# Performance work log

Measured on AMD Instinct MI355X. Metric: run time of the kernel, lower is better.

## Reference

```python
import jax, jax.numpy as jnp
import numpy as np

FEAT_STRIDE = 32  # 520 // 16
POOL = 7          # adaptive_avg_pool2d target (7,7)
C = 8             # channels consumed as (2 classes x 4 coords)


def setup_inputs() -> dict:
    key = jax.random.key(0)
    k1, k2, k3 = jax.random.split(key, 3)
    H = W = 1024
    conv_out = jax.random.normal(k1, (1, C, H, W), dtype=jnp.float32)
    n = 8192
    # sample pixel-space coords in [0, H*FEAT_STRIDE) and sort so min<=max per axis
    ys = jnp.sort(jax.random.randint(k2, (n, 2), 0, H * FEAT_STRIDE), axis=1)
    xs = jnp.sort(jax.random.randint(k3, (n, 2), 0, W * FEAT_STRIDE), axis=1)
    rois = jnp.stack([ys[:, 0], xs[:, 0], ys[:, 1], xs[:, 1]], axis=1).astype(jnp.int64)
    return {"conv_out": conv_out, "rois": rois}


def _adaptive_bounds(start, length):
    # PyTorch adaptive_avg_pool2d bin edges over [start, start+length)
    j = jnp.arange(POOL)
    lo = start + (j * length) // POOL
    hi = start + ((j + 1) * length + POOL - 1) // POOL  # ceil div
    return lo, hi


def _forward(conv_out, rois):
    r = rois // FEAT_STRIDE
    x = conv_out[0]  # [C, H, W]
    # summed-area table, padded so sat[:, y, x] = sum over [0:y, 0:x)
    sat = jnp.pad(jnp.cumsum(jnp.cumsum(x, axis=1), axis=2),
                  ((0, 0), (1, 0), (1, 0)))  # [C, H+1, W+1]

    def pool_one(roi):
        ymin, xmin = roi[0], roi[1]
        ymax, xmax = roi[2] + 1, roi[3] + 1  # exclusive ends
        ylo, yhi = _adaptive_bounds(ymin, ymax - ymin)
        xlo, xhi = _adaptive_bounds(xmin, xmax - xmin)
        # 7x7 bin sums via inclusion-exclusion on SAT -> [C,7,7]
        s = (sat[:, yhi[:, None], xhi[None, :]]
             - sat[:, ylo[:, None], xhi[None, :]]
             - sat[:, yhi[:, None], xlo[None, :]]
             + sat[:, ylo[:, None], xlo[None, :]])
        area = ((yhi - ylo)[:, None] * (xhi - xlo)[None, :]).astype(s.dtype)
        block7 = s / area                       # adaptive_avg_pool2d -> (7,7)
        return block7.mean(axis=(1, 2))         # adaptive_avg_pool2d -> (1,1), [C]

    pooled = jax.vmap(pool_one)(r)              # [n, C]
    return pooled.reshape(-1, 2, 4)


def reference(conv_out, rois):
    return _forward(conv_out, rois)
```

## Files before the change

### kernel.cpp

```cpp
#include <hip/hip_runtime.h>
#include <cstddef>
#include <cstdint>

#define SATW_PAD 1026
#define W8   8200
#define W8P  8208
#define NCH  8
#define STRIP 16
#define NSTRIP (W8P / STRIP)

__global__ __launch_bounds__(256) void rowscan_kernel(const float* __restrict__ in,
                                                      float* __restrict__ sat) {
    const int y    = blockIdx.x;
    const int t    = threadIdx.x;
    const int lane = t & 63;
    const int wv   = t >> 6;

    __shared__ float lds[NCH][1024];

    for (int k = 0; k < 2; ++k) {
        const int c = wv * 2 + k;
        const float4* r4 = (const float4*)(in + ((size_t)c * 1024 + y) * 1024);
        double chunkbase = 0.0;
#pragma unroll
        for (int j = 0; j < 4; ++j) {
            float4 a = r4[lane + 64 * j];
            double v0 = a.x, v1 = a.y, v2 = a.z, v3 = a.w;
            double s = v0 + v1 + v2 + v3;
            double ps = s;
#pragma unroll
            for (int off = 1; off < 64; off <<= 1) {
                double n = __shfl_up(ps, off, 64);
                if (lane >= off) ps += n;
            }
            double base = chunkbase + ps - s;
            double p0 = base + v0, p1 = p0 + v1, p2 = p1 + v2, p3 = p2 + v3;
            ((float4*)lds[c])[lane + 64 * j] =
                make_float4((float)p0, (float)p1, (float)p2, (float)p3);
            chunkbase += __shfl(ps, 63, 64);
        }
    }
    __syncthreads();

    float* orow = sat + (size_t)(y + 1) * W8P;
    for (int f4 = t; f4 < W8P / 4; f4 += 256) {
        int f = f4 * 4;
        float4 o;
        float* po = (float*)&o;
#pragma unroll
        for (int j = 0; j < 4; ++j) {
            int ff = f + j;
            int x = ff >> 3, c = ff & 7;
            po[j] = (x >= 1 && x <= 1024) ? lds[c][x - 1] : 0.0f;
        }
        ((float4*)orow)[f4] = o;
    }
}

__global__ __launch_bounds__(1024, 8) void colscan_block(float* __restrict__ sat) {
    const int t    = threadIdx.x;
    const int lane = t & 63;
    const int w    = t >> 6;
    const int rg   = lane >> 2;
    const int q    = lane & 3;
    const int c0   = blockIdx.x * STRIP + q * 4;

    float* p0 = sat + (size_t)(1 + w * 64 + rg * 4) * W8P + c0;

    float4 v[4];
#pragma unroll
    for (int k = 0; k < 4; ++k)
        v[k] = *(const float4*)(p0 + (size_t)k * W8P);

    double T0 = 0, T1 = 0, T2 = 0, T3 = 0;
#pragma unroll
    for (int k = 0; k < 4; ++k) {
        T0 += v[k].x; T1 += v[k].y; T2 += v[k].z; T3 += v[k].w;
    }

    double i0 = T0, i1 = T1, i2 = T2, i3 = T3;
#pragma unroll
    for (int s = 4; s <= 32; s <<= 1) {
        double a0 = __shfl_up(i0, s, 64), a1 = __shfl_up(i1, s, 64);
        double a2 = __shfl_up(i2, s, 64), a3 = __shfl_up(i3, s, 64);
        if (lane >= s) { i0 += a0; i1 += a1; i2 += a2; i3 += a3; }
    }
    double b0 = i0 - T0, b1 = i1 - T1, b2 = i2 - T2, b3 = i3 - T3;

    __shared__ double wt[16][4][4];
    if (lane >= 60) {
        wt[w][q][0] = i0; wt[w][q][1] = i1; wt[w][q][2] = i2; wt[w][q][3] = i3;
    }
    __syncthreads();
    for (int w2 = 0; w2 < w; ++w2) {
        b0 += wt[w2][q][0]; b1 += wt[w2][q][1];
        b2 += wt[w2][q][2]; b3 += wt[w2][q][3];
    }

#pragma unroll
    for (int k = 0; k < 4; ++k) {
        b0 += v[k].x; b1 += v[k].y; b2 += v[k].z; b3 += v[k].w;
        *(float4*)(p0 + (size_t)k * W8P) =
            make_float4((float)b0, (float)b1, (float)b2, (float)b3);
    }

    if (t < 4) {
        int cz = blockIdx.x * STRIP + t * 4;
        *(float4*)(sat + cz) = make_float4(0.f, 0.f, 0.f, 0.f);
    }
}

__global__ __launch_bounds__(256) void pool_kernel(const float* __restrict__ sat,
                                                   const int* __restrict__ rois,
                                                   float* __restrict__ out,
                                                   int n_roi) {
    int lane = threadIdx.x & 63;
    int roi  = (blockIdx.x * blockDim.x + threadIdx.x) >> 6;
    if (roi >= n_roi) return;

    const int4 rv = ((const int4*)rois)[roi];
    int ymin = rv.x >> 5;
    int xmin = rv.y >> 5;
    int Ly   = (rv.z >> 5) + 1 - ymin;
    int Lx   = (rv.w >> 5) + 1 - xmin;

    float acc[NCH];
#pragma unroll
    for (int c = 0; c < NCH; ++c) acc[c] = 0.0f;

    if (lane < 49) {
        int by = lane / 7;
        int bx = lane - by * 7;
        int ylo = ymin + (by * Ly) / 7;
        int yhi = ymin + ((by + 1) * Ly + 6) / 7;
        int xlo = xmin + (bx * Lx) / 7;
        int xhi = xmin + ((bx + 1) * Lx + 6) / 7;
        float inv = 1.0f / (float)((yhi - ylo) * (xhi - xlo));

        float4 a[2], b[2], c4[2], d[2];
        const float4* hh = (const float4*)(sat + ((size_t)yhi * SATW_PAD + xhi) * NCH);
        const float4* lh = (const float4*)(sat + ((size_t)ylo * SATW_PAD + xhi) * NCH);
        const float4* hl = (const float4*)(sat + ((size_t)yhi * SATW_PAD + xlo) * NCH);
        const float4* ll = (const float4*)(sat + ((size_t)ylo * SATW_PAD + xlo) * NCH);
        a[0] = hh[0]; a[1] = hh[1];
        b[0] = lh[0]; b[1] = lh[1];
        c4[0] = hl[0]; c4[1] = hl[1];
        d[0] = ll[0]; d[1] = ll[1];
        const float* fa = (const float*)a;
        const float* fb = (const float*)b;
        const float* fc = (const float*)c4;
        const float* fd = (const float*)d;
#pragma unroll
        for (int c = 0; c < NCH; ++c)
            acc[c] = (fa[c] - fb[c] - fc[c] + fd[c]) * inv;
    }

#pragma unroll
    for (int off = 32; off; off >>= 1) {
#pragma unroll
        for (int c = 0; c < NCH; ++c) acc[c] += __shfl_down(acc[c], off, 64);
    }

    if (lane == 0) {
        const float k = 1.0f / 49.0f;
        float4* po = (float4*)(out + (size_t)roi * NCH);
        po[0] = make_float4(acc[0] * k, acc[1] * k, acc[2] * k, acc[3] * k);
        po[1] = make_float4(acc[4] * k, acc[5] * k, acc[6] * k, acc[7] * k);
    }
}

extern "C" void kernel_launch(void* const* d_in, const int* in_sizes, int n_in,
                              void* d_out, int out_size, void* d_ws, size_t ws_size,
                              hipStream_t stream) {
    const float* conv = (const float*)d_in[0];
    const int*   rois = (const int*)d_in[1];
    float*       out  = (float*)d_out;
    int n_roi = in_sizes[1] / 4;

    float* sat = (float*)d_ws;

    rowscan_kernel<<<1024, 256, 0, stream>>>(conv, sat);
    colscan_block<<<NSTRIP, 1024, 0, stream>>>(sat);
    pool_kernel<<<(n_roi + 3) / 4, 256, 0, stream>>>(sat, rois, out, n_roi);
}
```

Measured before the change: 123.0 us.

## Replace column-scan kernel with three-pass band reduce/prefix/apply scan

```diff
diff --git a/kernel.cpp b/kernel.cpp
--- a/kernel.cpp
+++ b/kernel.cpp
@@ -1,13 +1,17 @@
 #include <hip/hip_runtime.h>
 #include <cstddef>
 #include <cstdint>
+
 
 #define SATW_PAD 1026
 #define W8   8200
 #define W8P  8208
 #define NCH  8
-#define STRIP 16
-#define NSTRIP (W8P / STRIP)
+
+#define NBAND 64
+#define BROWS 16
+#define CHUNK_F32 1024
+#define NCHUNK 9
 
 __global__ __launch_bounds__(256) void rowscan_kernel(const float* __restrict__ in,
                                                       float* __restrict__ sat) {
@@ -57,57 +61,98 @@
     }
 }
 
-__global__ __launch_bounds__(1024, 8) void colscan_block(float* __restrict__ sat) {
-    const int t    = threadIdx.x;
-    const int lane = t & 63;
-    const int w    = t >> 6;
-    const int rg   = lane >> 2;
-    const int q    = lane & 3;
-    const int c0   = blockIdx.x * STRIP + q * 4;
-
-    float* p0 = sat + (size_t)(1 + w * 64 + rg * 4) * W8P + c0;
-
-    float4 v[4];
-#pragma unroll
-    for (int k = 0; k < 4; ++k)
-        v[k] = *(const float4*)(p0 + (size_t)k * W8P);
-
-    double T0 = 0, T1 = 0, T2 = 0, T3 = 0;
-#pragma unroll
-    for (int k = 0; k < 4; ++k) {
-        T0 += v[k].x; T1 += v[k].y; T2 += v[k].z; T3 += v[k].w;
-    }
-
-    double i0 = T0, i1 = T1, i2 = T2, i3 = T3;
-#pragma unroll
-    for (int s = 4; s <= 32; s <<= 1) {
-        double a0 = __shfl_up(i0, s, 64), a1 = __shfl_up(i1, s, 64);
-        double a2 = __shfl_up(i2, s, 64), a3 = __shfl_up(i3, s, 64);
-        if (lane >= s) { i0 += a0; i1 += a1; i2 += a2; i3 += a3; }
-    }
-    double b0 = i0 - T0, b1 = i1 - T1, b2 = i2 - T2, b3 = i3 - T3;
-
-    __shared__ double wt[16][4][4];
-    if (lane >= 60) {
-        wt[w][q][0] = i0; wt[w][q][1] = i1; wt[w][q][2] = i2; wt[w][q][3] = i3;
-    }
-    __syncthreads();
-    for (int w2 = 0; w2 < w; ++w2) {
-        b0 += wt[w2][q][0]; b1 += wt[w2][q][1];
-        b2 += wt[w2][q][2]; b3 += wt[w2][q][3];
-    }
-
-#pragma unroll
-    for (int k = 0; k < 4; ++k) {
-        b0 += v[k].x; b1 += v[k].y; b2 += v[k].z; b3 += v[k].w;
-        *(float4*)(p0 + (size_t)k * W8P) =
-            make_float4((float)b0, (float)b1, (float)b2, (float)b3);
-    }
-
-    if (t < 4) {
-        int cz = blockIdx.x * STRIP + t * 4;
-        *(float4*)(sat + cz) = make_float4(0.f, 0.f, 0.f, 0.f);
-    }
+__global__ __launch_bounds__(256) void band_sum(const float* __restrict__ sat,
+                                                double* __restrict__ bsum) {
+    const int c = blockIdx.x;
+    const int b = blockIdx.y;
+    const int t = threadIdx.x;
+    const int col0 = c * CHUNK_F32 + t * 4;
+    if (col0 >= W8) return;
+
+    const float* p = sat + (size_t)(1 + b * BROWS) * W8P + col0;
+    float4 v[BROWS];
+#pragma unroll
+    for (int k = 0; k < BROWS; ++k)
+        v[k] = *(const float4*)(p + (size_t)k * W8P);
+
+    double s0 = 0, s1 = 0, s2 = 0, s3 = 0;
+#pragma unroll
+    for (int k = 0; k < BROWS; ++k) {
+        s0 += v[k].x; s1 += v[k].y; s2 += v[k].z; s3 += v[k].w;
+    }
+
+    double* o = bsum + (size_t)b * W8P + col0;
+    double2 lo, hi;
+    lo.x = s0; lo.y = s1; hi.x = s2; hi.y = s3;
+    *(double2*)o       = lo;
+    *((double2*)o + 1) = hi;
+}
+
+__global__ __launch_bounds__(64) void band_prefix(double* __restrict__ bsum) {
+    const int lane = threadIdx.x;
+    const int rg   = lane >> 3;
+    const int s    = lane & 7;
+    const size_t base = (size_t)blockIdx.x * 16 + (size_t)s * 2;
+
+    double2 v[8];
+#pragma unroll
+    for (int k = 0; k < 8; ++k)
+        v[k] = *(const double2*)(bsum + (size_t)(rg * 8 + k) * W8P + base);
+
+    double i0 = 0, i1 = 0;
+    double incl0[8], incl1[8];
+#pragma unroll
+    for (int k = 0; k < 8; ++k) {
+        i0 += v[k].x; i1 += v[k].y;
+        incl0[k] = i0; incl1[k] = i1;
+    }
+
+    double a0 = i0, a1 = i1;
+#pragma unroll
+    for (int off = 8; off <= 32; off <<= 1) {
+        double u0 = __shfl_up(a0, off, 64);
+        double u1 = __shfl_up(a1, off, 64);
+        if (lane >= off) { a0 += u0; a1 += u1; }
+    }
+    const double base0 = a0 - i0, base1 = a1 - i1;
+
+#pragma unroll
+    for (int k = 0; k < 8; ++k) {
+        double2 e;
+        e.x = base0 + incl0[k] - v[k].x;
+        e.y = base1 + incl1[k] - v[k].y;
+        *(double2*)(bsum + (size_t)(rg * 8 + k) * W8P + base) = e;
+    }
+}
+
+__global__ __launch_bounds__(256) void band_apply(float* __restrict__ sat,
+                                                  const double* __restrict__ bpre) {
+    const int c = blockIdx.x;
+    const int b = blockIdx.y;
+    const int t = threadIdx.x;
+    const int col0 = c * CHUNK_F32 + t * 4;
+    if (col0 >= W8) return;
+
+    const double* q = bpre + (size_t)b * W8P + col0;
+    double2 qlo = *(const double2*)q;
+    double2 qhi = *((const double2*)q + 1);
+    double a0 = qlo.x, a1 = qlo.y, a2 = qhi.x, a3 = qhi.y;
+
+    float* p = sat + (size_t)(1 + b * BROWS) * W8P + col0;
+    float4 v[BROWS];
+#pragma unroll
+    for (int k = 0; k < BROWS; ++k)
+        v[k] = *(const float4*)(p + (size_t)k * W8P);
+
+#pragma unroll
+    for (int k = 0; k < BROWS; ++k) {
+        a0 += v[k].x; a1 += v[k].y; a2 += v[k].z; a3 += v[k].w;
+        *(float4*)(p + (size_t)k * W8P) =
+            make_float4((float)a0, (float)a1, (float)a2, (float)a3);
+    }
+
+    if (b == 0)
+        *(float4*)(sat + col0) = make_float4(0.f, 0.f, 0.f, 0.f);
 }
 
 __global__ __launch_bounds__(256) void pool_kernel(const float* __restrict__ sat,
@@ -177,9 +222,12 @@
     float*       out  = (float*)d_out;
     int n_roi = in_sizes[1] / 4;
 
-    float* sat = (float*)d_ws;
+    float*  sat  = (float*)d_ws;
+    double* bsum = (double*)((char*)d_ws + 33652992);
 
     rowscan_kernel<<<1024, 256, 0, stream>>>(conv, sat);
-    colscan_block<<<NSTRIP, 1024, 0, stream>>>(sat);
+    band_sum   <<<dim3(NCHUNK, NBAND), 256, 0, stream>>>(sat, bsum);
+    band_prefix<<<513, 64, 0, stream>>>(bsum);
+    band_apply <<<dim3(NCHUNK, NBAND), 256, 0, stream>>>(sat, bsum);
     pool_kernel<<<(n_roi + 3) / 4, 256, 0, stream>>>(sat, rois, out, n_roi);
 }
```

Result: faster. 117.0 us (-4.9%).
